# Kernel tuning notes

Hardware: AMD Instinct MI355X
Metric: run time of the kernel (lower is better)

## Reference

```python
import jax, jax.numpy as jnp
import numpy as np

N_TAU = 10      # hardcoded in source (dt = tau / N_tau)
N_STEPS = 500   # N = floor(T/dt) with T=50, tau=1.0 -> dt=0.1
B, D, H = 1024, 128, 512


def setup_inputs() -> dict:
    key = jax.random.key(0)
    k0, k1, k2 = jax.random.split(key, 3)
    return {
        "x0": jax.random.normal(k0, (B, D), dtype=jnp.float32),
        "tau": jnp.ones((1,), dtype=jnp.float32),
        "W1": jax.random.normal(k1, (H, 2 * D + 1), dtype=jnp.float32) * (2 * D + 1) ** -0.5,
        "b1": jnp.zeros((H,), dtype=jnp.float32),
        "W2": jax.random.normal(k2, (D, H), dtype=jnp.float32) * H ** -0.5,
        "b2": jnp.zeros((D,), dtype=jnp.float32),
    }


def reference(x0, tau, W1, b1, W2, b2):
    """Forward-Euler DDE solve: x'(t) = F(x(t), x(t-tau), t), x(t)=x0 for t<=0.
    F(x, y, t) = W2 @ tanh(W1 @ [x; y; t] + b1) + b2, batched over B trajectories.
    Returns the trajectory with shape [N_STEPS+1, B, D]."""
    dt = tau[0] / N_TAU

    def F(x, y, t):
        # x, y: [B, D]; t: traced scalar
        tcol = jnp.full((x.shape[0], 1), 1.0, x.dtype) * t
        z = jnp.concatenate([x, y, tcol], axis=-1)          # [B, 2D+1]
        h = jnp.tanh(z @ W1.T + b1)                          # [B, H]
        return h @ W2.T + b2                                 # [B, D]

    # delay buffer: buf[0] = x_{n-N_tau} (delayed state), buf[-1] = x_n (current)
    buf0 = jnp.broadcast_to(x0, (N_TAU + 1,) + x0.shape)     # constant history X0

    def step(buf, n):
        t = n.astype(x0.dtype) * dt
        x_new = buf[-1] + dt * F(buf[-1], buf[0], t)
        buf = jnp.concatenate([buf[1:], x_new[None]], axis=0)
        return buf, x_new

    _, xs = jax.lax.scan(step, buf0, jnp.arange(N_STEPS))
    return jnp.concatenate([x0[None], xs], axis=0)           # [N+1, B, D]
```

## Files before the change

### kernel.cpp

```cpp
#include <hip/hip_runtime.h>

typedef float f32x4 __attribute__((ext_vector_type(4)));
typedef _Float16 f16x8 __attribute__((ext_vector_type(8)));

#define B_TOT   1024
#define D_DIM   128
#define H_DIM   512
#define N_STEPS 500
#define ROWS    4
#define WAVES   8

#define HSTRIDE 272
#define HSLOT   (8 * HSTRIDE)
#define BSTRIDE 1056
#define LDS_BOUNCE (11 * HSLOT)
#define LDS_TOTAL  (LDS_BOUNCE + 8 * BSTRIDE)

static __device__ __forceinline__ short f16b(float f) {
    _Float16 h = (_Float16)f;
    return __builtin_bit_cast(short, h);
}
static __device__ __forceinline__ float f16tof(short s) {
    return (float)__builtin_bit_cast(_Float16, s);
}
static __device__ __forceinline__ float tanh_fast(float x) {
    float e = __builtin_amdgcn_exp2f(x * 2.885390081777927f);
    return 1.0f - 2.0f * __builtin_amdgcn_rcpf(e + 1.0f);
}
static __device__ __forceinline__ f32x4 sx32(f32x4 v) {
    f32x4 r;
#pragma unroll
    for (int i = 0; i < 4; ++i) r[i] = __shfl_xor(v[i], 32);
    return r;
}
static __device__ __forceinline__ float pick(f32x4 v, int g) {
    float lo = (g & 1) ? v[1] : v[0];
    float hi = (g & 1) ? v[3] : v[2];
    return (g & 2) ? hi : lo;
}
static __device__ __forceinline__ void barrier_lds() {
    asm volatile("s_waitcnt lgkmcnt(0)" ::: "memory");
    __builtin_amdgcn_s_barrier();
}

__global__ __launch_bounds__(512)
__attribute__((amdgpu_waves_per_eu(2, 2)))
void ndde_kernel(
    const float* __restrict__ x0, const float* __restrict__ tau,
    const float* __restrict__ W1, const float* __restrict__ b1,
    const float* __restrict__ W2, const float* __restrict__ b2,
    float* __restrict__ out)
{
    __shared__ __align__(16) char smem[LDS_TOTAL];

    const int tid = threadIdx.x;
    const int w   = tid >> 6;
    const int l   = tid & 63;
    const int g   = l >> 4;
    const int l15 = l & 15;
    const int ur  = (l15 & 3) | ((l15 >> 3) << 2);
    const int r0  = blockIdx.x * ROWS;
    const int d   = 16 * w + l15;

    const float dtv = tau[0] * 0.1f;

    f16x8 w1f[4][8];
    f16x8 w2f[16];
    float b1f[4], w1tf[4];

#pragma unroll
    for (int nt = 0; nt < 4; ++nt) {
        const int hr = 64 * w + 16 * nt + l15;
        const float* wr = W1 + (long)hr * 257;
#pragma unroll
        for (int ks = 0; ks < 8; ++ks) {
            const int c0 = 32 * ks + 8 * g;
            f16x8 f;
#pragma unroll
            for (int j = 0; j < 8; ++j) f[j] = (_Float16)wr[c0 + j];
            w1f[nt][ks] = f;
        }
        b1f[nt]  = b1[hr];
        w1tf[nt] = wr[256];
    }
    {
        const float* wr = W2 + (long)d * 512;
#pragma unroll
        for (int ks = 0; ks < 16; ++ks) {
            const int c0 = 32 * ks + 8 * g;
            f16x8 f;
#pragma unroll
            for (int j = 0; j < 8; ++j) f[j] = (_Float16)wr[c0 + j];
            w2f[ks] = f;
        }
    }
    const float b2v = b2[d];
    float xo = x0[(long)(r0 + g) * D_DIM + d];

    {
        short hb = f16b(xo);
        short lb = f16b(xo - f16tof(hb));
        for (int s = 0; s < 11; ++s) {
            *(short*)(smem + s * HSLOT + g * HSTRIDE + 2 * d)       = hb;
            *(short*)(smem + s * HSLOT + (g + 4) * HSTRIDE + 2 * d) = lb;
        }
        out[(long)(r0 + g) * D_DIM + d] = xo;
    }
    __syncthreads();

    const int histRd   = ur * HSTRIDE + 16 * g;
    const int bounceRd = LDS_BOUNCE + ur * BSTRIDE + ((16 * g) ^ ((ur & 3) << 4));
    const int bwXor    = g << 4;

    float* po = out + (long)(B_TOT * D_DIM) + (long)(r0 + g) * D_DIM + d;

    int cur = 0;
    int ys  = 1;

    f32x4 accY[4];
#pragma unroll
    for (int nt = 0; nt < 4; ++nt) accY[nt] = (f32x4){0.f, 0.f, 0.f, 0.f};
    {
        const char* yb = smem + 1 * HSLOT + histRd;
#pragma unroll
        for (int ks = 0; ks < 4; ++ks) {
            f16x8 ya = *(const f16x8*)(yb + 64 * ks);
#pragma unroll
            for (int nt = 0; nt < 4; ++nt)
                accY[nt] = __builtin_amdgcn_mfma_f32_16x16x32_f16(ya, w1f[nt][ks + 4], accY[nt], 0, 0, 0);
        }
    }

#pragma clang loop unroll(disable)
    for (int n = 0; n < N_STEPS; ++n) {
        const float t = (float)n * dtv;

        const char* xb = smem + cur * HSLOT + histRd;
#pragma unroll
        for (int ks = 0; ks < 4; ++ks) {
            f16x8 xa = *(const f16x8*)(xb + 64 * ks);
#pragma unroll
            for (int nt = 0; nt < 4; ++nt)
                accY[nt] = __builtin_amdgcn_mfma_f32_16x16x32_f16(xa, w1f[nt][ks], accY[nt], 0, 0, 0);
        }

#pragma unroll
        for (int nt = 0; nt < 4; ++nt) {
            f32x4 c = accY[nt];
            c += sx32(c);
            float hp = pick(c, g) + fmaf(t, w1tf[nt], b1f[nt]);
            float h  = tanh_fast(hp);
            short hh = f16b(h);
            short hl = f16b(h - f16tof(hh));
            const int cb = (2 * (64 * w + 16 * nt + l15)) ^ bwXor;
            *(short*)(smem + LDS_BOUNCE + g * BSTRIDE + cb)       = hh;
            *(short*)(smem + LDS_BOUNCE + (g + 4) * BSTRIDE + cb) = hl;
        }
        barrier_lds();

        f32x4 a2c[4];
#pragma unroll
        for (int c = 0; c < 4; ++c) {
            a2c[c] = (f32x4){0.f, 0.f, 0.f, 0.f};
#pragma unroll
            for (int k = 0; k < 4; ++k) {
                f16x8 ha = *(const f16x8*)(smem + bounceRd + 64 * (4 * c + k));
                a2c[c] = __builtin_amdgcn_mfma_f32_16x16x32_f16(ha, w2f[4 * c + k], a2c[c], 0, 0, 0);
            }
        }

        const int ysN = (ys == 10) ? 0 : ys + 1;
#pragma unroll
        for (int nt = 0; nt < 4; ++nt) accY[nt] = (f32x4){0.f, 0.f, 0.f, 0.f};
        {
            const char* yb = smem + ysN * HSLOT + histRd;
#pragma unroll
            for (int ks = 0; ks < 4; ++ks) {
                f16x8 ya = *(const f16x8*)(yb + 64 * ks);
#pragma unroll
                for (int nt = 0; nt < 4; ++nt)
                    accY[nt] = __builtin_amdgcn_mfma_f32_16x16x32_f16(ya, w1f[nt][ks + 4], accY[nt], 0, 0, 0);
            }
        }

        f32x4 acc2 = (a2c[0] + a2c[1]) + (a2c[2] + a2c[3]);
        acc2 += sx32(acc2);
        const float o  = pick(acc2, g) + b2v;
        const float xn = fmaf(dtv, o, xo);
        xo = xn;
        {
            short hb = f16b(xn);
            short lb = f16b(xn - f16tof(hb));
            *(short*)(smem + ys * HSLOT + g * HSTRIDE + 2 * d)       = hb;
            *(short*)(smem + ys * HSLOT + (g + 4) * HSTRIDE + 2 * d) = lb;
        }
        __builtin_nontemporal_store(xn, po);
        po += B_TOT * D_DIM;

        cur = ys;
        ys  = ysN;
        barrier_lds();
    }
}

extern "C" void kernel_launch(void* const* d_in, const int* in_sizes, int n_in,
                              void* d_out, int out_size, void* d_ws, size_t ws_size,
                              hipStream_t stream) {
    (void)in_sizes; (void)n_in; (void)out_size; (void)d_ws; (void)ws_size;
    const float* x0  = (const float*)d_in[0];
    const float* tau = (const float*)d_in[1];
    const float* W1  = (const float*)d_in[2];
    const float* b1  = (const float*)d_in[3];
    const float* W2  = (const float*)d_in[4];
    const float* b2  = (const float*)d_in[5];
    float* out = (float*)d_out;

    ndde_kernel<<<dim3(B_TOT / ROWS), dim3(64 * WAVES), 0, stream>>>(
        x0, tau, W1, b1, W2, b2, out);
}
```

Baseline: 939.5 us.

## Reorder hi/lo split rows so MFMA partial sums reduce in-lane without shuffles

Changes the row layout of the fp16 hi/lo-split history and hidden bounce buffers so that each lane's MFMA accumulator holds both the hi and lo partial sums for two batch rows. The sums then combine with plain in-register adds, replacing the cross-lane shfl_xor(32) and select logic after both GEMMs. Only the lower half of each wave (l < 32) writes LDS and global output, and the bounce-buffer swizzle changes to match. The intent is to take cross-lane traffic off the serial per-step critical path, at the cost of running tanh twice per lane and leaving half the lanes idle during stores.

```diff
diff --git a/kernel.cpp b/kernel.cpp
--- a/kernel.cpp
+++ b/kernel.cpp
@@ -5,7 +5,6 @@
 
 #define B_TOT   1024
 #define D_DIM   128
-#define H_DIM   512
 #define N_STEPS 500
 #define ROWS    4
 #define WAVES   8
@@ -26,17 +25,6 @@
 static __device__ __forceinline__ float tanh_fast(float x) {
     float e = __builtin_amdgcn_exp2f(x * 2.885390081777927f);
     return 1.0f - 2.0f * __builtin_amdgcn_rcpf(e + 1.0f);
-}
-static __device__ __forceinline__ f32x4 sx32(f32x4 v) {
-    f32x4 r;
-#pragma unroll
-    for (int i = 0; i < 4; ++i) r[i] = __shfl_xor(v[i], 32);
-    return r;
-}
-static __device__ __forceinline__ float pick(f32x4 v, int g) {
-    float lo = (g & 1) ? v[1] : v[0];
-    float hi = (g & 1) ? v[3] : v[2];
-    return (g & 2) ? hi : lo;
 }
 static __device__ __forceinline__ void barrier_lds() {
     asm volatile("s_waitcnt lgkmcnt(0)" ::: "memory");
@@ -58,9 +46,13 @@
     const int l   = tid & 63;
     const int g   = l >> 4;
     const int l15 = l & 15;
-    const int ur  = (l15 & 3) | ((l15 >> 3) << 2);
+    const int hs  = (l >> 4) & 1;
+    const int bb  = 2 * hs;
+    const bool act = (l < 32);
     const int r0  = blockIdx.x * ROWS;
     const int d   = 16 * w + l15;
+    const int rb  = tid >> 7;
+    const int rd  = tid & 127;
 
     const float dtv = tau[0] * 0.1f;
 
@@ -95,24 +87,30 @@
         }
     }
     const float b2v = b2[d];
-    float xo = x0[(long)(r0 + g) * D_DIM + d];
+    float xo0 = x0[(long)(r0 + bb)     * D_DIM + d];
+    float xo1 = x0[(long)(r0 + bb + 1) * D_DIM + d];
 
     {
-        short hb = f16b(xo);
-        short lb = f16b(xo - f16tof(hb));
+        float v = x0[(long)(r0 + rb) * D_DIM + rd];
+        short hb = f16b(v);
+        short lb = f16b(v - f16tof(hb));
         for (int s = 0; s < 11; ++s) {
-            *(short*)(smem + s * HSLOT + g * HSTRIDE + 2 * d)       = hb;
-            *(short*)(smem + s * HSLOT + (g + 4) * HSTRIDE + 2 * d) = lb;
-        }
-        out[(long)(r0 + g) * D_DIM + d] = xo;
+            char* sl = smem + s * HSLOT;
+            *(short*)(sl + (2 * rb)     * HSTRIDE + 2 * rd) = hb;
+            *(short*)(sl + (2 * rb + 1) * HSTRIDE + 2 * rd) = lb;
+        }
+        out[(long)(r0 + rb) * D_DIM + rd] = v;
     }
     __syncthreads();
 
-    const int histRd   = ur * HSTRIDE + 16 * g;
-    const int bounceRd = LDS_BOUNCE + ur * BSTRIDE + ((16 * g) ^ ((ur & 3) << 4));
-    const int bwXor    = g << 4;
-
-    float* po = out + (long)(B_TOT * D_DIM) + (long)(r0 + g) * D_DIM + d;
+    const int hrw     = l15 & 7;
+    const int histRd  = hrw * HSTRIDE + 16 * g;
+    const int bounceRd = LDS_BOUNCE + hrw * BSTRIDE
+                       + ((16 * g) ^ (((hrw >> 2) & 1) << 5));
+    const int xrw     = hs << 5;
+    const int brow0   = 4 * hs;
+
+    float* po0 = out + (long)(B_TOT * D_DIM) + (long)(r0 + bb) * D_DIM + d;
 
     int cur = 0;
     int ys  = 1;
@@ -146,15 +144,21 @@
 
 #pragma unroll
         for (int nt = 0; nt < 4; ++nt) {
-            f32x4 c = accY[nt];
-            c += sx32(c);
-            float hp = pick(c, g) + fmaf(t, w1tf[nt], b1f[nt]);
-            float h  = tanh_fast(hp);
-            short hh = f16b(h);
-            short hl = f16b(h - f16tof(hh));
-            const int cb = (2 * (64 * w + 16 * nt + l15)) ^ bwXor;
-            *(short*)(smem + LDS_BOUNCE + g * BSTRIDE + cb)       = hh;
-            *(short*)(smem + LDS_BOUNCE + (g + 4) * BSTRIDE + cb) = hl;
+            float sb = fmaf(t, w1tf[nt], b1f[nt]);
+            float h0 = tanh_fast(accY[nt][0] + accY[nt][1] + sb);
+            float h1 = tanh_fast(accY[nt][2] + accY[nt][3] + sb);
+            short h0h = f16b(h0);
+            short h0l = f16b(h0 - f16tof(h0h));
+            short h1h = f16b(h1);
+            short h1l = f16b(h1 - f16tof(h1h));
+            if (act) {
+                const int cb = (2 * (64 * w + 16 * nt + l15)) ^ xrw;
+                char* base = smem + LDS_BOUNCE;
+                *(short*)(base + (brow0 + 0) * BSTRIDE + cb) = h0h;
+                *(short*)(base + (brow0 + 1) * BSTRIDE + cb) = h0l;
+                *(short*)(base + (brow0 + 2) * BSTRIDE + cb) = h1h;
+                *(short*)(base + (brow0 + 3) * BSTRIDE + cb) = h1l;
+            }
         }
         barrier_lds();
 
@@ -184,18 +188,24 @@
         }
 
         f32x4 acc2 = (a2c[0] + a2c[1]) + (a2c[2] + a2c[3]);
-        acc2 += sx32(acc2);
-        const float o  = pick(acc2, g) + b2v;
-        const float xn = fmaf(dtv, o, xo);
-        xo = xn;
-        {
-            short hb = f16b(xn);
-            short lb = f16b(xn - f16tof(hb));
-            *(short*)(smem + ys * HSLOT + g * HSTRIDE + 2 * d)       = hb;
-            *(short*)(smem + ys * HSLOT + (g + 4) * HSTRIDE + 2 * d) = lb;
-        }
-        __builtin_nontemporal_store(xn, po);
-        po += B_TOT * D_DIM;
+        const float xn0 = fmaf(dtv, (acc2[0] + acc2[1]) + b2v, xo0);
+        const float xn1 = fmaf(dtv, (acc2[2] + acc2[3]) + b2v, xo1);
+        xo0 = xn0;
+        xo1 = xn1;
+        if (act) {
+            short h0h = f16b(xn0);
+            short h0l = f16b(xn0 - f16tof(h0h));
+            short h1h = f16b(xn1);
+            short h1l = f16b(xn1 - f16tof(h1h));
+            char* sl = smem + ys * HSLOT + 2 * d;
+            *(short*)(sl + (2 * bb)     * HSTRIDE) = h0h;
+            *(short*)(sl + (2 * bb + 1) * HSTRIDE) = h0l;
+            *(short*)(sl + (2 * bb + 2) * HSTRIDE) = h1h;
+            *(short*)(sl + (2 * bb + 3) * HSTRIDE) = h1l;
+            __builtin_nontemporal_store(xn0, po0);
+            __builtin_nontemporal_store(xn1, po0 + D_DIM);
+        }
+        po0 += B_TOT * D_DIM;
 
         cur = ys;
         ys  = ysN;
```

New measurement: 895.1 us. 1.05x faster.
